# Optimization experiments

Measured on AMD Instinct MI355X. Metric: run time of the kernel, lower is better.

## Reference

```python
import math
import jax, jax.numpy as jnp
import numpy as np

# ---- Clifford algebra Cl(1,3) tables (static, built in numpy) ----
DIM = 4
METRIC = np.array([1.0, -1.0, -1.0, -1.0], dtype=np.float64)
N_COMP = 1 << DIM  # 16 multivector components
SUBSPACES = np.array([math.comb(DIM, g) for g in range(DIM + 1)])  # [1,4,6,4,1]

def _popcount(x):
    return bin(x).count("1")

# blades ordered by (grade, bitmask) as in CGENN-style algebras
_BLADES = sorted(range(N_COMP), key=lambda b: (_popcount(b), b))
_IDX = {b: i for i, b in enumerate(_BLADES)}

def _blade_prod(a, b):
    # canonical reordering sign
    s, t = 0, a >> 1
    while t:
        s += _popcount(t & b)
        t >>= 1
    sign = -1.0 if (s % 2) else 1.0
    for i in range(DIM):
        if (a >> i) & 1 and (b >> i) & 1:
            sign *= METRIC[i]
    return a ^ b, sign

# cayley[i, j, k]: coefficient of e_j in e_i * e_k  (matches einsum '...i,ijk,...k->...j')
CAYLEY = np.zeros((N_COMP, N_COMP, N_COMP), dtype=np.float32)
for a in range(N_COMP):
    for b in range(N_COMP):
        c, s = _blade_prod(a, b)
        CAYLEY[_IDX[a], _IDX[c], _IDX[b]] = s

GRADES = np.array([_popcount(b) for b in _BLADES])
BETA = np.array([float(np.prod([METRIC[i] for i in range(DIM) if (b >> i) & 1])) for b in _BLADES], dtype=np.float32)  # blade quadratic-form signs
GRADE_ONEHOT = (GRADES[:, None] == np.arange(DIM + 1)[None, :]).astype(np.float32)  # [16,5]

_sl = np.concatenate([[0], np.cumsum(SUBSPACES)])
PATHS = np.zeros((DIM + 1,) * 3, dtype=bool)
for i in range(DIM + 1):
    for j in range(DIM + 1):
        for k in range(DIM + 1):
            PATHS[i, j, k] = np.any(CAYLEY[_sl[i]:_sl[i+1], _sl[j]:_sl[j+1], _sl[k]:_sl[k+1]] != 0)
PI, PJ, PK = np.nonzero(PATHS)
N_PATHS = int(PATHS.sum())  # 35 for Cl(1,3)
EPS = 1e-6


def mvlinear(x, w):
    # x: [b, m, 16], w: [n, m, 5] (one scalar weight per grade) -> [b, n, 16]
    w16 = jnp.repeat(w, SUBSPACES, axis=-1)  # [n, m, 16]
    return jnp.einsum('bmi,nmi->bni', x, w16)


def normalize(x, a):
    # per-grade norm: |b(x_g, x_g)|^0.5, gated by sigmoid(a)
    q = ((x * x) * BETA) @ GRADE_ONEHOT            # [b, n, 5]
    norms = jnp.sqrt(jnp.abs(q))
    norms = jax.nn.sigmoid(a) * (norms - 1.0) + 1.0
    norms16 = jnp.repeat(norms, SUBSPACES, axis=-1)  # [b, n, 16]
    return x / (norms16 + EPS)


def get_weight(gp_weight):
    # scatter [F, 35] params into [F,5,5,5], expand to [F,16,16,16], mask by Cayley
    F = gp_weight.shape[0]
    w = jnp.zeros((F, DIM + 1, DIM + 1, DIM + 1), gp_weight.dtype).at[:, PI, PJ, PK].set(gp_weight)
    w = jnp.repeat(w, SUBSPACES, axis=1)
    w = jnp.repeat(w, SUBSPACES, axis=2)
    w = jnp.repeat(w, SUBSPACES, axis=3)
    return jnp.asarray(CAYLEY) * w  # [F,16,16,16]


def setup_inputs() -> dict:
    key = jax.random.key(0)
    k0, k1, k2, k3, k4 = jax.random.split(key, 5)
    B, F = 4096, 512
    x = jax.random.normal(k0, (B, F, N_COMP), jnp.float32)
    s = 1.0 / math.sqrt(F)
    w_left = jax.random.normal(k1, (F, F, DIM + 1), jnp.float32) * s
    b_left = jax.random.normal(k2, (F,), jnp.float32) * 0.01
    w_right = jax.random.normal(k3, (F, F, DIM + 1), jnp.float32) * s
    a_norm = jnp.zeros((F, DIM + 1), jnp.float32)  # normalization_init = 0
    gp_weight = jax.random.normal(k4, (F, N_PATHS), jnp.float32) * (1.0 / math.sqrt(DIM + 1))
    return {"x": x, "w_left": w_left, "b_left": b_left, "w_right": w_right,
            "a_norm": a_norm, "gp_weight": gp_weight}


def reference(x, w_left, b_left, w_right, a_norm, gp_weight):
    input_right = normalize(mvlinear(x, w_right), a_norm)
    W = get_weight(gp_weight)                       # [F,16,16,16]
    gp = jnp.einsum('bni,nijk,bnk->bnj', x, W, input_right)
    left = mvlinear(x, w_left).at[..., 0].add(b_left)  # bias embedded at grade-0 component
    return (left + gp) / math.sqrt(2.0)
```

## Files before the change

kernel.cpp:

```cpp
#include <hip/hip_runtime.h>

typedef unsigned int uint;
typedef unsigned short ushort;
typedef __attribute__((ext_vector_type(8))) short bf16x8;
typedef __attribute__((ext_vector_type(4))) float f32x4;

struct GPTables {
    signed char jid[16][16];
    float       sgn[16][16];
    signed char pid[16][16];
    float       beta[16];
    signed char grade[16];
};

constexpr int popc4(int x) { return ((x >> 0) & 1) + ((x >> 1) & 1) + ((x >> 2) & 1) + ((x >> 3) & 1); }

constexpr GPTables make_tables() {
    GPTables T{};
    int blades[16] = {0, 1, 2, 4, 8, 3, 5, 6, 9, 10, 12, 7, 11, 13, 14, 15};
    int idxof[16] = {};
    for (int i = 0; i < 16; ++i) idxof[blades[i]] = i;
    float metric[4] = {1.f, -1.f, -1.f, -1.f};
    for (int i = 0; i < 16; ++i) {
        T.grade[i] = (signed char)popc4(blades[i]);
        float b = 1.f;
        for (int bit = 0; bit < 4; ++bit)
            if ((blades[i] >> bit) & 1) b *= metric[bit];
        T.beta[i] = b;
    }
    bool paths[5][5][5] = {};
    for (int a = 0; a < 16; ++a)
        for (int b = 0; b < 16; ++b)
            paths[popc4(a)][popc4(a ^ b)][popc4(b)] = true;
    int pid3[5][5][5] = {};
    int cnt = 0;
    for (int gi = 0; gi < 5; ++gi)
        for (int gj = 0; gj < 5; ++gj)
            for (int gk = 0; gk < 5; ++gk)
                if (paths[gi][gj][gk]) pid3[gi][gj][gk] = cnt++;
    for (int ii = 0; ii < 16; ++ii) {
        for (int kk = 0; kk < 16; ++kk) {
            int a = blades[ii], b = blades[kk];
            int c = a ^ b;
            int s = 0, t = a >> 1;
            while (t) { s += popc4(t & b); t >>= 1; }
            float sign = (s & 1) ? -1.f : 1.f;
            for (int bit = 0; bit < 4; ++bit)
                if (((a >> bit) & 1) && ((b >> bit) & 1)) sign *= metric[bit];
            T.jid[ii][kk] = (signed char)idxof[c];
            T.sgn[ii][kk] = sign;
            T.pid[ii][kk] = (signed char)pid3[popc4(a)][popc4(c)][popc4(b)];
        }
    }
    return T;
}

constexpr GPTables TBL = make_tables();

#define BF (4096)
#define FF (512)
#define BM_ (2097152)
#define FFFF (262144)

__device__ inline ushort f2bf(float f) {
    uint u = __float_as_uint(f);
    uint r = (u + 0x7fffu + ((u >> 16) & 1u)) >> 16;
    return (ushort)r;
}
__device__ inline float bf2f(ushort h) { return __uint_as_float(((uint)h) << 16); }

typedef __attribute__((address_space(3))) uint lds_u32;
typedef const __attribute__((address_space(1))) uint g_u32;
__device__ __forceinline__ void gload16(const void* gsrc, void* ldst) {
    __builtin_amdgcn_global_load_lds((g_u32*)gsrc, (lds_u32*)ldst, 16, 0, 0);
}

__global__ __launch_bounds__(256) void k_transpose_x(const float* __restrict__ x,
                                                     ushort* __restrict__ Xh,
                                                     ushort* __restrict__ Xl) {
    const int p0 = (blockIdx.x * 256 + threadIdx.x) * 2;
    float v[32];
    const float4* x4 = (const float4*)(x + (size_t)p0 * 16);
#pragma unroll
    for (int j = 0; j < 8; ++j) {
        float4 t = x4[j];
        v[j * 4 + 0] = t.x; v[j * 4 + 1] = t.y; v[j * 4 + 2] = t.z; v[j * 4 + 3] = t.w;
    }
#pragma unroll
    for (int i = 0; i < 16; ++i) {
        ushort h0 = f2bf(v[i]),      h1 = f2bf(v[16 + i]);
        ushort l0 = f2bf(v[i] - bf2f(h0));
        ushort l1 = f2bf(v[16 + i] - bf2f(h1));
        *(uint*)&Xh[(size_t)i * BM_ + p0] = (uint)h0 | ((uint)h1 << 16);
        *(uint*)&Xl[(size_t)i * BM_ + p0] = (uint)l0 | ((uint)l1 << 16);
    }
}

__global__ __launch_bounds__(256) void k_prep_w(const float* __restrict__ w_right,
                                                const float* __restrict__ w_left,
                                                ushort* __restrict__ Wb) {
    const int n = blockIdx.x;
    const int m = threadIdx.x * 2;
#pragma unroll
    for (int g = 0; g < 5; ++g) {
        float a = w_right[(size_t)n * (FF * 5) + (size_t)m * 5 + g];
        float b = w_right[(size_t)n * (FF * 5) + (size_t)(m + 1) * 5 + g];
        ushort ah = f2bf(a), bh = f2bf(b);
        ushort al = f2bf(a - bf2f(ah)), bl = f2bf(b - bf2f(bh));
        *(uint*)&Wb[(size_t)g * FFFF + (size_t)n * FF + m] = (uint)ah | ((uint)bh << 16);
        *(uint*)&Wb[(size_t)(5 + g) * FFFF + (size_t)n * FF + m] = (uint)al | ((uint)bl << 16);
        float c = w_left[(size_t)n * (FF * 5) + (size_t)m * 5 + g];
        float d = w_left[(size_t)n * (FF * 5) + (size_t)(m + 1) * 5 + g];
        *(uint*)&Wb[(size_t)(10 + g) * FFFF + (size_t)n * FF + m] =
            (uint)f2bf(c) | ((uint)f2bf(d) << 16);
    }
}

__device__ __forceinline__ bf16x8 ldfrag(const ushort* tile, int row, int colb) {
    return *(const bf16x8*)((const char*)tile + row * 64 + (colb ^ (((row >> 2) & 3) << 4)));
}

__global__ __launch_bounds__(256, 2) void k_gemm(const ushort* __restrict__ Xh,
                                                 const ushort* __restrict__ Xl,
                                                 const ushort* __restrict__ Wb,
                                                 float* __restrict__ OutR,
                                                 ushort* __restrict__ OutL) {
    const int comp = blockIdx.z;
    const int g = TBL.grade[comp];
    const ushort* Ah = Xh + (size_t)comp * BM_;
    const ushort* Al = Xl + (size_t)comp * BM_;
    const ushort* Bh = Wb + (size_t)g * FFFF;
    const ushort* Bl = Wb + (size_t)(5 + g) * FFFF;
    const ushort* BL = Wb + (size_t)(10 + g) * FFFF;
    const int m0 = blockIdx.x * 128;
    const int n0 = blockIdx.y * 128;

    __shared__ ushort sh[2 * 5 * 4096];

    const int tid = threadIdx.x;
    const int lane = tid & 63, wid = tid >> 6;
    const int wm = wid >> 1, wn = wid & 1;
    const int lr = lane & 15;
    const int kb = (lane >> 4) * 16;

    const size_t mb_ = (size_t)m0 * (FF * 2), nb_ = (size_t)n0 * (FF * 2);

    auto stage = [&](int buf, int k0) {
#pragma unroll
        for (int pass = 0; pass < 2; ++pass) {
            const int c = tid + pass * 256;
            const int row = c >> 2;
            const int scb = ((c & 3) * 16) ^ (((c >> 4) & 3) << 4);
            const size_t gb = (size_t)row * (FF * 2) + (size_t)k0 * 2 + scb;
            char* dst = (char*)sh + buf * 40960 + c * 16;
            gload16((const char*)Ah + mb_ + gb, dst);
            gload16((const char*)Al + mb_ + gb, dst + 8192);
            gload16((const char*)Bh + nb_ + gb, dst + 16384);
            gload16((const char*)Bl + nb_ + gb, dst + 24576);
            gload16((const char*)BL + nb_ + gb, dst + 32768);
        }
    };

    f32x4 accR[4][4] = {};
    f32x4 accL[4][4] = {};

    stage(0, 0);
    __syncthreads();

    for (int t = 0; t < 16; ++t) {
        const ushort* sb = sh + (t & 1) * 20480;
        if (t < 15) stage((t + 1) & 1, (t + 1) * 32);

        const ushort* tA  = sb;
        const ushort* tAl = sb + 1 * 4096;
        const ushort* tBh = sb + 2 * 4096;
        const ushort* tBl = sb + 3 * 4096;
        const ushort* tBL = sb + 4 * 4096;

        bf16x8 ah[4], al[4], bh[4], bl[4], bLf[4];
#pragma unroll
        for (int mb = 0; mb < 4; ++mb) {
            ah[mb] = ldfrag(tA,  wm * 64 + mb * 16 + lr, kb);
            al[mb] = ldfrag(tAl, wm * 64 + mb * 16 + lr, kb);
        }
#pragma unroll
        for (int nb = 0; nb < 4; ++nb) {
            bh[nb]  = ldfrag(tBh, wn * 64 + nb * 16 + lr, kb);
            bl[nb]  = ldfrag(tBl, wn * 64 + nb * 16 + lr, kb);
            bLf[nb] = ldfrag(tBL, wn * 64 + nb * 16 + lr, kb);
        }
#pragma unroll
        for (int mb = 0; mb < 4; ++mb)
#pragma unroll
            for (int nb = 0; nb < 4; ++nb) {
                accR[mb][nb] = __builtin_amdgcn_mfma_f32_16x16x32_bf16(ah[mb], bh[nb],  accR[mb][nb], 0, 0, 0);
                accR[mb][nb] = __builtin_amdgcn_mfma_f32_16x16x32_bf16(ah[mb], bl[nb],  accR[mb][nb], 0, 0, 0);
                accR[mb][nb] = __builtin_amdgcn_mfma_f32_16x16x32_bf16(al[mb], bh[nb],  accR[mb][nb], 0, 0, 0);
                accL[mb][nb] = __builtin_amdgcn_mfma_f32_16x16x32_bf16(ah[mb], bLf[nb], accL[mb][nb], 0, 0, 0);
            }
        __syncthreads();
    }

    float* CR = OutR + (size_t)comp * BM_;
    ushort* CL = OutL + (size_t)comp * BM_;
#pragma unroll
    for (int mb = 0; mb < 4; ++mb)
#pragma unroll
        for (int nb = 0; nb < 4; ++nb) {
            int row = m0 + wm * 64 + mb * 16 + (lane >> 4) * 4;
            int col = n0 + wn * 64 + nb * 16 + (lane & 15);
#pragma unroll
            for (int r = 0; r < 4; ++r) {
                CR[(size_t)(row + r) * FF + col] = accR[mb][nb][r];
                CL[(size_t)(row + r) * FF + col] = f2bf(accL[mb][nb][r]);
            }
        }
}

__global__ __launch_bounds__(256) void k_gp(const float* __restrict__ x,
                                            const float* __restrict__ OutR,
                                            const ushort* __restrict__ OutL,
                                            const float* __restrict__ gpw,
                                            const float* __restrict__ a_norm,
                                            const float* __restrict__ b_left,
                                            float* __restrict__ out) {
    __shared__ float s_pw[256 * 35];
    __shared__ float s_an[256 * 5];
    __shared__ float s_bl[256];

    const int tid = threadIdx.x;
    const int bn = blockIdx.x * 256 + tid;
    const int n0 = (blockIdx.x & 1) * 256;

    for (int i = tid; i < 256 * 35; i += 256) s_pw[i] = gpw[(size_t)n0 * 35 + i];
#pragma unroll
    for (int i = 0; i < 5; ++i) s_an[tid + i * 256] = a_norm[(size_t)n0 * 5 + tid + i * 256];
    s_bl[tid] = b_left[n0 + tid];
    __syncthreads();

    float xi[16];
    {
        const float4* xp = (const float4*)(x + (size_t)bn * 16);
#pragma unroll
        for (int j = 0; j < 4; ++j) {
            float4 t = xp[j];
            xi[j * 4 + 0] = t.x; xi[j * 4 + 1] = t.y; xi[j * 4 + 2] = t.z; xi[j * 4 + 3] = t.w;
        }
    }

    float R[16];
#pragma unroll
    for (int i = 0; i < 16; ++i) R[i] = OutR[(size_t)i * BM_ + bn];

    float q[5] = {0.f, 0.f, 0.f, 0.f, 0.f};
#pragma unroll
    for (int i = 0; i < 16; ++i) q[TBL.grade[i]] += TBL.beta[i] * R[i] * R[i];
    float inv[5];
#pragma unroll
    for (int g = 0; g < 5; ++g) {
        float nr = sqrtf(fabsf(q[g]));
        float a = s_an[tid * 5 + g];
        float sig = 1.f / (1.f + __expf(-a));
        float nf = sig * (nr - 1.f) + 1.f + 1e-6f;
        inv[g] = 1.f / nf;
    }
#pragma unroll
    for (int i = 0; i < 16; ++i) R[i] *= inv[TBL.grade[i]];

    float pw[35];
#pragma unroll
    for (int p = 0; p < 35; ++p) pw[p] = s_pw[tid * 35 + p];

    float acc[16] = {};
#pragma unroll
    for (int ii = 0; ii < 16; ++ii) {
#pragma unroll
        for (int kk = 0; kk < 16; ++kk) {
            const int j = TBL.jid[ii][kk];
            const int p = TBL.pid[ii][kk];
            const float s = TBL.sgn[ii][kk];
            acc[j] += (s * pw[p]) * (xi[ii] * R[kk]);
        }
    }

    const float bl = s_bl[tid];
    float o[16];
#pragma unroll
    for (int j = 0; j < 16; ++j) {
        float l = bf2f(OutL[(size_t)j * BM_ + bn]);
        if (j == 0) l += bl;
        o[j] = (l + acc[j]) * 0.70710678118654752440f;
    }
    float4* op = (float4*)(out + (size_t)bn * 16);
#pragma unroll
    for (int j = 0; j < 4; ++j) {
        float4 t;
        t.x = o[j * 4 + 0]; t.y = o[j * 4 + 1]; t.z = o[j * 4 + 2]; t.w = o[j * 4 + 3];
        op[j] = t;
    }
}

extern "C" void kernel_launch(void* const* d_in, const int* in_sizes, int n_in,
                              void* d_out, int out_size, void* d_ws, size_t ws_size,
                              hipStream_t stream) {
    (void)in_sizes; (void)n_in; (void)out_size; (void)ws_size;
    const float* x       = (const float*)d_in[0];
    const float* w_left  = (const float*)d_in[1];
    const float* b_left  = (const float*)d_in[2];
    const float* w_right = (const float*)d_in[3];
    const float* a_norm  = (const float*)d_in[4];
    const float* gpw     = (const float*)d_in[5];
    float* out = (float*)d_out;

    char* ws = (char*)d_ws;
    ushort* Xh   = (ushort*)ws;
    ushort* Xl   = (ushort*)(ws + 67108864);
    ushort* Wb   = (ushort*)(ws + 134217728);
    float*  OutR = (float*)(ws + 142082048);
    ushort* OutL = (ushort*)(ws + 276299776);

    k_transpose_x<<<4096, 256, 0, stream>>>(x, Xh, Xl);
    k_prep_w<<<512, 256, 0, stream>>>(w_right, w_left, Wb);
    dim3 g(32, 4, 16);
    k_gemm<<<g, 256, 0, stream>>>(Xh, Xl, Wb, OutR, OutL);
    k_gp<<<8192, 256, 0, stream>>>(x, OutR, OutL, gpw, a_norm, b_left, out);
}
```

Measured before the change: 350.6 us.

## Load GEMM B fragments directly from global, shrink LDS, transpose gp tables

The GEMM now stages only the A (hi/lo) tiles through LDS and reads the three B weight fragments straight from global memory into registers. This cuts LDS use from 80KB to 32KB, and the occupancy hint is raised from 2 to 4 blocks. The geometric-product kernel no longer copies gp weights and norm params into LDS; a small prep kernel (launched after the GEMM) writes transposed gp weights and precomputed sigmoids so each thread loads them coalesced from global. The risk is uncoalesced, latency-exposed global loads for B inside the MFMA loop, and the prep kernel reuses workspace that overlaps Xh, which is safe only because it runs after the GEMM has consumed it.

Measured after the change: 1.147 ms. 227% more time.

```diff
diff --git a/kernel.cpp b/kernel.cpp
--- a/kernel.cpp
+++ b/kernel.cpp
@@ -116,11 +116,23 @@
     }
 }
 
+__global__ __launch_bounds__(256) void k_prep_tables(const float* __restrict__ gpw,
+                                                     const float* __restrict__ a_norm,
+                                                     float* __restrict__ gpwT,
+                                                     float* __restrict__ sigT) {
+    const int n = blockIdx.x * 256 + threadIdx.x;
+#pragma unroll
+    for (int p = 0; p < 35; ++p) gpwT[(size_t)p * FF + n] = gpw[(size_t)n * 35 + p];
+#pragma unroll
+    for (int g = 0; g < 5; ++g)
+        sigT[(size_t)g * FF + n] = 1.f / (1.f + __expf(-a_norm[(size_t)n * 5 + g]));
+}
+
 __device__ __forceinline__ bf16x8 ldfrag(const ushort* tile, int row, int colb) {
     return *(const bf16x8*)((const char*)tile + row * 64 + (colb ^ (((row >> 2) & 3) << 4)));
 }
 
-__global__ __launch_bounds__(256, 2) void k_gemm(const ushort* __restrict__ Xh,
+__global__ __launch_bounds__(256, 4) void k_gemm(const ushort* __restrict__ Xh,
                                                  const ushort* __restrict__ Xl,
                                                  const ushort* __restrict__ Wb,
                                                  float* __restrict__ OutR,
@@ -135,15 +147,17 @@
     const int m0 = blockIdx.x * 128;
     const int n0 = blockIdx.y * 128;
 
-    __shared__ ushort sh[2 * 5 * 4096];
+    __shared__ ushort sh[2 * 2 * 4096];
 
     const int tid = threadIdx.x;
     const int lane = tid & 63, wid = tid >> 6;
     const int wm = wid >> 1, wn = wid & 1;
     const int lr = lane & 15;
-    const int kb = (lane >> 4) * 16;
-
-    const size_t mb_ = (size_t)m0 * (FF * 2), nb_ = (size_t)n0 * (FF * 2);
+    const int kh = lane >> 4;
+    const int kb = kh * 16;
+
+    const size_t mb_ = (size_t)m0 * (FF * 2);
+    const int nrow = n0 + wn * 64 + lr;
 
     auto stage = [&](int buf, int k0) {
 #pragma unroll
@@ -152,12 +166,9 @@
             const int row = c >> 2;
             const int scb = ((c & 3) * 16) ^ (((c >> 4) & 3) << 4);
             const size_t gb = (size_t)row * (FF * 2) + (size_t)k0 * 2 + scb;
-            char* dst = (char*)sh + buf * 40960 + c * 16;
+            char* dst = (char*)sh + buf * 16384 + c * 16;
             gload16((const char*)Ah + mb_ + gb, dst);
             gload16((const char*)Al + mb_ + gb, dst + 8192);
-            gload16((const char*)Bh + nb_ + gb, dst + 16384);
-            gload16((const char*)Bl + nb_ + gb, dst + 24576);
-            gload16((const char*)BL + nb_ + gb, dst + 32768);
         }
     };
 
@@ -168,35 +179,34 @@
     __syncthreads();
 
     for (int t = 0; t < 16; ++t) {
-        const ushort* sb = sh + (t & 1) * 20480;
-        if (t < 15) stage((t + 1) & 1, (t + 1) * 32);
-
-        const ushort* tA  = sb;
-        const ushort* tAl = sb + 1 * 4096;
-        const ushort* tBh = sb + 2 * 4096;
-        const ushort* tBl = sb + 3 * 4096;
-        const ushort* tBL = sb + 4 * 4096;
-
-        bf16x8 ah[4], al[4], bh[4], bl[4], bLf[4];
+        const int k0 = t * 32;
+
+        bf16x8 bh[4], bl4[4], bL4[4];
+#pragma unroll
+        for (int nb = 0; nb < 4; ++nb) {
+            const size_t off = (size_t)(nrow + nb * 16) * FF + k0 + kh * 8;
+            bh[nb]  = *(const bf16x8*)(Bh + off);
+            bl4[nb] = *(const bf16x8*)(Bl + off);
+            bL4[nb] = *(const bf16x8*)(BL + off);
+        }
+
+        if (t < 15) stage((t + 1) & 1, k0 + 32);
+
+        const ushort* sb = sh + (t & 1) * 8192;
+        bf16x8 ah[4], al[4];
 #pragma unroll
         for (int mb = 0; mb < 4; ++mb) {
-            ah[mb] = ldfrag(tA,  wm * 64 + mb * 16 + lr, kb);
-            al[mb] = ldfrag(tAl, wm * 64 + mb * 16 + lr, kb);
-        }
-#pragma unroll
-        for (int nb = 0; nb < 4; ++nb) {
-            bh[nb]  = ldfrag(tBh, wn * 64 + nb * 16 + lr, kb);
-            bl[nb]  = ldfrag(tBl, wn * 64 + nb * 16 + lr, kb);
-            bLf[nb] = ldfrag(tBL, wn * 64 + nb * 16 + lr, kb);
+            ah[mb] = ldfrag(sb,        wm * 64 + mb * 16 + lr, kb);
+            al[mb] = ldfrag(sb + 4096, wm * 64 + mb * 16 + lr, kb);
         }
 #pragma unroll
         for (int mb = 0; mb < 4; ++mb)
 #pragma unroll
             for (int nb = 0; nb < 4; ++nb) {
                 accR[mb][nb] = __builtin_amdgcn_mfma_f32_16x16x32_bf16(ah[mb], bh[nb],  accR[mb][nb], 0, 0, 0);
-                accR[mb][nb] = __builtin_amdgcn_mfma_f32_16x16x32_bf16(ah[mb], bl[nb],  accR[mb][nb], 0, 0, 0);
+                accR[mb][nb] = __builtin_amdgcn_mfma_f32_16x16x32_bf16(ah[mb], bl4[nb], accR[mb][nb], 0, 0, 0);
                 accR[mb][nb] = __builtin_amdgcn_mfma_f32_16x16x32_bf16(al[mb], bh[nb],  accR[mb][nb], 0, 0, 0);
-                accL[mb][nb] = __builtin_amdgcn_mfma_f32_16x16x32_bf16(ah[mb], bLf[nb], accL[mb][nb], 0, 0, 0);
+                accL[mb][nb] = __builtin_amdgcn_mfma_f32_16x16x32_bf16(ah[mb], bL4[nb], accL[mb][nb], 0, 0, 0);
             }
         __syncthreads();
     }
@@ -220,23 +230,17 @@
 __global__ __launch_bounds__(256) void k_gp(const float* __restrict__ x,
                                             const float* __restrict__ OutR,
                                             const ushort* __restrict__ OutL,
-                                            const float* __restrict__ gpw,
-                                            const float* __restrict__ a_norm,
+                                            const float* __restrict__ gpwT,
+                                            const float* __restrict__ sigT,
                                             const float* __restrict__ b_left,
                                             float* __restrict__ out) {
-    __shared__ float s_pw[256 * 35];
-    __shared__ float s_an[256 * 5];
-    __shared__ float s_bl[256];
-
     const int tid = threadIdx.x;
     const int bn = blockIdx.x * 256 + tid;
-    const int n0 = (blockIdx.x & 1) * 256;
-
-    for (int i = tid; i < 256 * 35; i += 256) s_pw[i] = gpw[(size_t)n0 * 35 + i];
-#pragma unroll
-    for (int i = 0; i < 5; ++i) s_an[tid + i * 256] = a_norm[(size_t)n0 * 5 + tid + i * 256];
-    s_bl[tid] = b_left[n0 + tid];
-    __syncthreads();
+    const int n = bn & (FF - 1);
+
+    float pw[35];
+#pragma unroll
+    for (int p = 0; p < 35; ++p) pw[p] = gpwT[(size_t)p * FF + n];
 
     float xi[16];
     {
@@ -259,17 +263,12 @@
 #pragma unroll
     for (int g = 0; g < 5; ++g) {
         float nr = sqrtf(fabsf(q[g]));
-        float a = s_an[tid * 5 + g];
-        float sig = 1.f / (1.f + __expf(-a));
+        float sig = sigT[(size_t)g * FF + n];
         float nf = sig * (nr - 1.f) + 1.f + 1e-6f;
         inv[g] = 1.f / nf;
     }
 #pragma unroll
     for (int i = 0; i < 16; ++i) R[i] *= inv[TBL.grade[i]];
-
-    float pw[35];
-#pragma unroll
-    for (int p = 0; p < 35; ++p) pw[p] = s_pw[tid * 35 + p];
 
     float acc[16] = {};
 #pragma unroll
@@ -283,7 +282,7 @@
         }
     }
 
-    const float bl = s_bl[tid];
+    const float bl = b_left[n];
     float o[16];
 #pragma unroll
     for (int j = 0; j < 16; ++j) {
@@ -318,10 +317,13 @@
     ushort* Wb   = (ushort*)(ws + 134217728);
     float*  OutR = (float*)(ws + 142082048);
     ushort* OutL = (ushort*)(ws + 276299776);
+    float*  gpwT = (float*)ws;
+    float*  sigT = (float*)(ws + 71680);
 
     k_transpose_x<<<4096, 256, 0, stream>>>(x, Xh, Xl);
     k_prep_w<<<512, 256, 0, stream>>>(w_right, w_left, Wb);
     dim3 g(32, 4, 16);
     k_gemm<<<g, 256, 0, stream>>>(Xh, Xl, Wb, OutR, OutL);
-    k_gp<<<8192, 256, 0, stream>>>(x, OutR, OutL, gpw, a_norm, b_left, out);
-}
+    k_prep_tables<<<2, 256, 0, stream>>>(gpw, a_norm, gpwT, sigT);
+    k_gp<<<8192, 256, 0, stream>>>(x, OutR, OutL, gpwT, sigT, b_left, out);
+}
```
